# Kernel optimization log

Hardware: AMD Instinct MI355X
Metric: run time of the kernel (lower is better)

Reference implementation:

```python
import jax, jax.numpy as jnp
import numpy as np

# ---- configuration matching init_kwargs ----
KH, KW = 3, 3
STRIDE = (1, 1)
PAD = (1, 1)
DIL = (1, 1)
GRID_SIZE = 5
SPLINE_ORDER = 3
GRID_RANGE = (-1.0, 1.0)
CIN, COUT = 16, 32
B, H, W = 16, 64, 64
K = KH * KW                      # in_features of each KANLinear
NB = GRID_SIZE + SPLINE_ORDER    # number of B-spline basis functions / coeffs


def make_grid():
    # efficient-KAN style extended uniform knot vector, shared by all units
    h = (GRID_RANGE[1] - GRID_RANGE[0]) / GRID_SIZE
    return (jnp.arange(-SPLINE_ORDER, GRID_SIZE + SPLINE_ORDER + 1,
                       dtype=jnp.float32) * h + GRID_RANGE[0])  # [G + 2k + 1]


def setup_inputs() -> dict:
    key = jax.random.key(0)
    k1, k2, k3, k4 = jax.random.split(key, 4)
    n_convs = COUT * CIN  # one KANLinear per (out_channel, in_channel) pair
    x = jax.random.normal(k1, (B, CIN, H, W), dtype=jnp.float32)
    base_w = jax.random.normal(k2, (n_convs, K), dtype=jnp.float32) * (1.0 / np.sqrt(K))
    spline_w = jax.random.normal(k3, (n_convs, K, NB), dtype=jnp.float32) * 0.1
    spline_scaler = jax.random.normal(k4, (n_convs, K), dtype=jnp.float32) * (1.0 / np.sqrt(K))
    return {"x": x, "base_w": base_w, "spline_w": spline_w,
            "spline_scaler": spline_scaler}


def extract_patches(x):
    # im2col / torch.nn.Unfold: [B, Cin, H, W] -> [B, Cin, Ho, Wo, K]
    xp = jnp.pad(x, ((0, 0), (0, 0), (PAD[0], PAD[0]), (PAD[1], PAD[1])))
    Hp, Wp = xp.shape[2], xp.shape[3]
    Ho = (Hp - DIL[0] * (KH - 1) - 1) // STRIDE[0] + 1
    Wo = (Wp - DIL[1] * (KW - 1) - 1) // STRIDE[1] + 1
    cols = []
    for i in range(KH):          # tiny fixed kernel loop (9 iters)
        for j in range(KW):
            cols.append(xp[:, :,
                           i * DIL[0]: i * DIL[0] + STRIDE[0] * Ho: STRIDE[0],
                           j * DIL[1]: j * DIL[1] + STRIDE[1] * Wo: STRIDE[1]])
    return jnp.stack(cols, axis=-1)  # [B, Cin, Ho, Wo, K]


def bspline_bases(x, t):
    # Cox-de Boor recursion, vectorized over all leading dims.
    # x: [...], t: [G+2k+1] shared knots -> bases [..., NB]
    xe = x[..., None]
    b = ((xe >= t[:-1]) & (xe < t[1:])).astype(x.dtype)
    for p in range(1, SPLINE_ORDER + 1):
        left = (xe - t[:-(p + 1)]) / (t[p:-1] - t[:-(p + 1)]) * b[..., :-1]
        right = (t[p + 1:] - xe) / (t[p + 1:] - t[1:-p]) * b[..., 1:]
        b = left + right
    return b  # [..., NB]


def reference(x, base_w, spline_w, spline_scaler):
    t = make_grid()
    patches = extract_patches(x)                 # [B, Cin, Ho, Wo, K]
    act = jax.nn.silu(patches)                   # base branch activation
    bases = bspline_bases(patches, t)            # [B, Cin, Ho, Wo, K, NB]
    # KANLinear list ordering: kernel index = c_out * Cin + c_in
    bw = base_w.reshape(COUT, CIN, K)
    sw = (spline_w * spline_scaler[..., None]).reshape(COUT, CIN, K, NB)
    # out[b,o,h,w] = sum_i KANLinear_{o,i}(patch[b,i,h,w,:])
    out = jnp.einsum('bihwk,oik->bohw', act, bw)
    out = out + jnp.einsum('bihwkc,oikc->bohw', bases, sw)
    return out
```

## Files before the change

### kernel.cpp

```cpp
#include <hip/hip_runtime.h>
#include <hip/hip_bf16.h>

#define CIN_ 16
#define COUT_ 32
#define NBATCH_ 16
#define H_ 64
#define W_ 64
#define F_ 9
#define LPIX_ 304
#define PXT_ 34
#define LROWT_ (PXT_ * LPIX_)
#define ROWS_ 6
#define NSITE_ (ROWS_ * PXT_)
#define NIT_ 13

typedef __attribute__((ext_vector_type(8))) short short8;
typedef __attribute__((ext_vector_type(4))) float f32x4;
typedef __attribute__((ext_vector_type(16))) float f32x16;

__device__ __forceinline__ unsigned short f2bf(float f) {
    unsigned u = __builtin_bit_cast(unsigned, f);
    u += 0x7FFFu + ((u >> 16) & 1u);
    return (unsigned short)(u >> 16);
}
__device__ __forceinline__ unsigned pack2(float lo, float hi) {
    return (unsigned)f2bf(lo) | ((unsigned)f2bf(hi) << 16);
}

__global__ void kan_packw(const float* __restrict__ bw, const float* __restrict__ sw,
                          const float* __restrict__ sc, unsigned short* __restrict__ wpk) {
    int e = blockIdx.x * 256 + threadIdx.x;
    if (e >= 32 * 16 * 9) return;
    int n = e / 144;
    int ci = (e / 9) & 15;
    int tap = e % 9;
    float bwv = bw[e];
    float scv = sc[e];
    float4 s0 = *(const float4*)(sw + (size_t)e * 8);
    float4 s1 = *(const float4*)(sw + (size_t)e * 8 + 4);
    float swv[8] = {s0.x, s0.y, s0.z, s0.w, s1.x, s1.y, s1.z, s1.w};
#pragma unroll
    for (int f = 0; f < 9; ++f) {
        float v = (f == 0) ? bwv : swv[f - 1] * scv;
        int k = ci * 9 + f;
        int step = k >> 4, r = k & 15;
        int lane = ((r >> 3) << 5) | n;
        int j = r & 7;
        wpk[((size_t)(tap * 9 + step) * 64 + lane) * 8 + j] = f2bf(v);
    }
}

__global__ __launch_bounds__(256, 2) void kan_fused(const float* __restrict__ x,
                                                    const unsigned short* __restrict__ wpk,
                                                    float* __restrict__ out) {
    __shared__ __align__(16) char lA[ROWS_ * LROWT_];
    int tid = threadIdx.x;
    int bb = blockIdx.x >> 5;
    int rem = blockIdx.x & 31;
    int rg = rem >> 1;
    int wseg = rem & 1;
    int h0 = rg * 4;
    int w0 = wseg * 32;

    {
        int ci = tid >> 4;
        int l = tid & 15;
        const float* xb = x + ((size_t)bb * CIN_ + ci) * (H_ * W_);
        float xr[NIT_];
#pragma unroll
        for (int it = 0; it < NIT_; ++it) {
            int s = it * 16 + l;
            int r = s / PXT_;
            int lpx = s - r * PXT_;
            int hy = h0 + r - 1;
            int wx = w0 + lpx - 1;
            bool v = (s < NSITE_) && (hy >= 0) && (hy < H_) && (wx >= 0) && (wx < W_);
            xr[it] = v ? xb[hy * W_ + wx] : 0.f;
        }
#pragma unroll
        for (int it = 0; it < NIT_; ++it) {
            int s = it * 16 + l;
            if (s < NSITE_) {
                int r = s / PXT_;
                int lpx = s - r * PXT_;
                float xv = xr[it];
                float ua = (xv + 2.2f) * 2.5f;
                float mf = floorf(ua);
                float u = ua - mf;
                bool ok = (ua >= 0.0f) && (ua < 11.0f);
                float u2 = u * u, u3 = u2 * u;
                const float c6 = 1.0f / 6.0f;
                float Bm  = u3 * c6;
                float Bm1 = (-3.f * u3 + 3.f * u2 + 3.f * u + 1.f) * c6;
                float Bm2 = (3.f * u3 - 6.f * u2 + 4.f) * c6;
                float om = 1.f - u;
                float Bm3 = om * om * om * c6;
                unsigned P0 = pack2(Bm3, Bm2);
                unsigned P1 = pack2(Bm1, Bm);
                int sh = ok ? ((int)mf - 2) : 99;
                int a = sh >> 1;
                bool odd = sh & 1;
                unsigned Q0 = odd ? (P0 << 16) : P0;
                unsigned Q1 = odd ? ((P0 >> 16) | (P1 << 16)) : P1;
                unsigned Q2 = odd ? (P1 >> 16) : 0u;
                unsigned wq[5];
#pragma unroll
                for (int q = 0; q < 5; ++q)
                    wq[q] = (q == a) ? Q0 : (q == a + 1) ? Q1 : (q == a + 2) ? Q2 : 0u;
                float sil = xv / (1.f + __expf(-xv));
                wq[0] = (wq[0] & 0xFFFF0000u) | (unsigned)f2bf(sil);
                char* base = lA + r * LROWT_ + lpx * LPIX_ + ci * 18;
                if ((ci & 1) == 0) {
                    unsigned* d32 = (unsigned*)base;
#pragma unroll
                    for (int q = 0; q < 4; ++q) d32[q] = wq[q];
                    ((unsigned short*)base)[8] = (unsigned short)wq[4];
                } else {
                    ((unsigned short*)base)[0] = (unsigned short)wq[0];
                    unsigned* d32 = (unsigned*)(base + 2);
#pragma unroll
                    for (int q = 0; q < 4; ++q)
                        d32[q] = (wq[q] >> 16) | (wq[q + 1] << 16);
                }
            }
        }
    }

    int lane = tid & 63, wv = tid >> 6;

    short8 B[2][9];
#pragma unroll
    for (int s = 0; s < 9; ++s)
        B[0][s] = *(const short8*)(wpk + ((size_t)s * 64 + lane) * 8);

    __syncthreads();

    f32x16 acc = {};

#pragma unroll
    for (int tap = 0; tap < 9; ++tap) {
        int cur = tap & 1, nxt = cur ^ 1;
        if (tap < 8) {
#pragma unroll
            for (int s = 0; s < 9; ++s)
                B[nxt][s] = *(const short8*)(wpk +
                    ((size_t)((tap + 1) * 9 + s) * 64 + lane) * 8);
        }
        int ki = tap / 3, kj = tap - ki * 3;
        const char* abase = lA + (wv + ki) * LROWT_ + ((lane & 31) + kj) * LPIX_ +
                            ((lane >> 5) << 4);
        __builtin_amdgcn_s_setprio(1);
#pragma unroll
        for (int s = 0; s < 9; ++s) {
            short8 av = *(const short8*)(abase + s * 32);
            acc = __builtin_amdgcn_mfma_f32_32x32x16_bf16(av, B[cur][s], acc, 0, 0, 0);
        }
        __builtin_amdgcn_s_setprio(0);
    }

    int ch = lane & 31;
    int hh = h0 + wv;
    float* ob = out + (size_t)bb * COUT_ * (H_ * W_) + (size_t)ch * (H_ * W_) +
                (size_t)hh * W_ + w0;
#pragma unroll
    for (int q = 0; q < 4; ++q) {
        int px0 = q * 8 + ((lane >> 5) << 2);
        f32x4 v = {acc[q * 4 + 0], acc[q * 4 + 1], acc[q * 4 + 2], acc[q * 4 + 3]};
        __builtin_nontemporal_store(v, (f32x4*)(ob + px0));
    }
}

__device__ __forceinline__ void kan_feat_ref(float xv, float* f) {
    float ua = (xv + 2.2f) * 2.5f;
    float mf = floorf(ua);
    int m = (int)mf;
    float u = ua - mf;
    bool ok = (ua >= 0.0f) && (ua < 11.0f);
    float u2 = u * u, u3 = u2 * u;
    const float c6 = 1.0f / 6.0f;
    float Bm  = u3 * c6;
    float Bm1 = (-3.f * u3 + 3.f * u2 + 3.f * u + 1.f) * c6;
    float Bm2 = (3.f * u3 - 6.f * u2 + 4.f) * c6;
    float om = 1.f - u;
    float Bm3 = om * om * om * c6;
    if (!ok) { Bm = 0.f; Bm1 = 0.f; Bm2 = 0.f; Bm3 = 0.f; }
    f[0] = xv / (1.f + __expf(-xv));
#pragma unroll
    for (int j = 0; j < 8; ++j) {
        float v = 0.f;
        v = (m == j)     ? Bm  : v;
        v = (m == j + 1) ? Bm1 : v;
        v = (m == j + 2) ? Bm2 : v;
        v = (m == j + 3) ? Bm3 : v;
        f[1 + j] = v;
    }
}

__global__ void kan_direct(const float* __restrict__ x, const float* __restrict__ bw,
                           const float* __restrict__ sw, const float* __restrict__ sc,
                           float* __restrict__ out) {
    int idx = blockIdx.x * 256 + threadIdx.x;
    if (idx >= NBATCH_ * COUT_ * H_ * W_) return;
    int w = idx & 63, hh = (idx >> 6) & 63, o = (idx >> 12) & 31, b = idx >> 17;
    float acc = 0.0f;
    for (int i = 0; i < CIN_; ++i)
        for (int ki = 0; ki < 3; ++ki)
            for (int kj = 0; kj < 3; ++kj) {
                int hy = hh + ki - 1, wx = w + kj - 1;
                float xv = (hy >= 0 && hy < H_ && wx >= 0 && wx < W_)
                               ? x[(((size_t)b * CIN_ + i) * H_ + hy) * W_ + wx]
                               : 0.0f;
                float f[9];
                kan_feat_ref(xv, f);
                int idx9 = (o * CIN_ + i) * 9 + ki * 3 + kj;
                float a = f[0] * bw[idx9];
                float s = sc[idx9];
#pragma unroll
                for (int cc = 0; cc < 8; ++cc) a += f[1 + cc] * sw[idx9 * 8 + cc] * s;
                acc += a;
            }
    out[idx] = acc;
}

extern "C" void kernel_launch(void* const* d_in, const int* in_sizes, int n_in,
                              void* d_out, int out_size, void* d_ws, size_t ws_size,
                              hipStream_t stream) {
    const float* x  = (const float*)d_in[0];
    const float* bw = (const float*)d_in[1];
    const float* sw = (const float*)d_in[2];
    const float* sc = (const float*)d_in[3];
    float* out = (float*)d_out;

    size_t need = (size_t)9 * 9 * 64 * 8 * 2;
    if (ws_size >= need) {
        unsigned short* wpk = (unsigned short*)d_ws;
        kan_packw<<<dim3(18), 256, 0, stream>>>(bw, sw, sc, wpk);
        kan_fused<<<dim3(NBATCH_ * 32), 256, 0, stream>>>(x, wpk, out);
    } else {
        kan_direct<<<dim3((NBATCH_ * COUT_ * H_ * W_ + 255) / 256), 256, 0, stream>>>(
            x, bw, sw, sc, out);
    }
}
```

Measured before the change: 21.90 us.

## Fuse weight packing into main kernel with flag-based grid sync and padded features

```diff
diff --git a/kernel.cpp b/kernel.cpp
--- a/kernel.cpp
+++ b/kernel.cpp
@@ -6,13 +6,17 @@
 #define NBATCH_ 16
 #define H_ 64
 #define W_ 64
-#define F_ 9
-#define LPIX_ 304
+#define F_ 10
+#define LPIX_ 336
 #define PXT_ 34
 #define LROWT_ (PXT_ * LPIX_)
 #define ROWS_ 6
 #define NSITE_ (ROWS_ * PXT_)
 #define NIT_ 13
+#define NPACK_ 18
+#define NTILE_ 512
+#define MAGIC_ 0x5EEDF00Du
+#define WPKSH_ (9 * 10 * 64 * 8)
 
 typedef __attribute__((ext_vector_type(8))) short short8;
 typedef __attribute__((ext_vector_type(4))) float f32x4;
@@ -27,40 +31,50 @@
     return (unsigned)f2bf(lo) | ((unsigned)f2bf(hi) << 16);
 }
 
-__global__ void kan_packw(const float* __restrict__ bw, const float* __restrict__ sw,
-                          const float* __restrict__ sc, unsigned short* __restrict__ wpk) {
-    int e = blockIdx.x * 256 + threadIdx.x;
-    if (e >= 32 * 16 * 9) return;
-    int n = e / 144;
-    int ci = (e / 9) & 15;
-    int tap = e % 9;
-    float bwv = bw[e];
-    float scv = sc[e];
-    float4 s0 = *(const float4*)(sw + (size_t)e * 8);
-    float4 s1 = *(const float4*)(sw + (size_t)e * 8 + 4);
-    float swv[8] = {s0.x, s0.y, s0.z, s0.w, s1.x, s1.y, s1.z, s1.w};
-#pragma unroll
-    for (int f = 0; f < 9; ++f) {
-        float v = (f == 0) ? bwv : swv[f - 1] * scv;
-        int k = ci * 9 + f;
-        int step = k >> 4, r = k & 15;
-        int lane = ((r >> 3) << 5) | n;
-        int j = r & 7;
-        wpk[((size_t)(tap * 9 + step) * 64 + lane) * 8 + j] = f2bf(v);
-    }
-}
-
-__global__ __launch_bounds__(256, 2) void kan_fused(const float* __restrict__ x,
-                                                    const unsigned short* __restrict__ wpk,
-                                                    float* __restrict__ out) {
+__global__ __launch_bounds__(256, 2) void kan_one(const float* __restrict__ x,
+                                                  const float* __restrict__ bw,
+                                                  const float* __restrict__ sw,
+                                                  const float* __restrict__ sc,
+                                                  unsigned short* __restrict__ wpk,
+                                                  unsigned* __restrict__ flags,
+                                                  float* __restrict__ out) {
     __shared__ __align__(16) char lA[ROWS_ * LROWT_];
     int tid = threadIdx.x;
-    int bb = blockIdx.x >> 5;
-    int rem = blockIdx.x & 31;
-    int rg = rem >> 1;
-    int wseg = rem & 1;
-    int h0 = rg * 4;
-    int w0 = wseg * 32;
+    int pid = blockIdx.x;
+
+    if (pid < NPACK_) {
+        int e = pid * 256 + tid;
+        if (e < 32 * 16 * 9) {
+            int n = e / 144;
+            int ci = (e / 9) & 15;
+            int tap = e % 9;
+            float bwv = bw[e];
+            float scv = sc[e];
+            float4 s0 = *(const float4*)(sw + (size_t)e * 8);
+            float4 s1 = *(const float4*)(sw + (size_t)e * 8 + 4);
+            float swv[8] = {s0.x, s0.y, s0.z, s0.w, s1.x, s1.y, s1.z, s1.w};
+#pragma unroll
+            for (int f = 0; f < 10; ++f) {
+                float v = (f == 0) ? bwv : (f <= 8 ? swv[f - 1] * scv : 0.0f);
+                int k = ci * 10 + f;
+                int step = k >> 4, r = k & 15;
+                int lane = ((r >> 3) << 5) | n;
+                int j = r & 7;
+                wpk[((size_t)(tap * 10 + step) * 64 + lane) * 8 + j] = f2bf(v);
+            }
+        }
+        __threadfence();
+        __syncthreads();
+        if (tid == 0)
+            __hip_atomic_store(&flags[pid], MAGIC_, __ATOMIC_RELEASE,
+                               __HIP_MEMORY_SCOPE_AGENT);
+    }
+
+    int tile = (pid < NPACK_) ? (NTILE_ - NPACK_ + pid) : (pid - NPACK_);
+    int bb = tile >> 5;
+    int rem = tile & 31;
+    int h0 = (rem >> 1) * 4;
+    int w0 = (rem & 1) * 32;
 
     {
         int ci = tid >> 4;
@@ -107,51 +121,50 @@
 #pragma unroll
                 for (int q = 0; q < 5; ++q)
                     wq[q] = (q == a) ? Q0 : (q == a + 1) ? Q1 : (q == a + 2) ? Q2 : 0u;
-                float sil = xv / (1.f + __expf(-xv));
+                float sil = xv * __builtin_amdgcn_rcpf(1.f + __expf(-xv));
                 wq[0] = (wq[0] & 0xFFFF0000u) | (unsigned)f2bf(sil);
-                char* base = lA + r * LROWT_ + lpx * LPIX_ + ci * 18;
-                if ((ci & 1) == 0) {
-                    unsigned* d32 = (unsigned*)base;
-#pragma unroll
-                    for (int q = 0; q < 4; ++q) d32[q] = wq[q];
-                    ((unsigned short*)base)[8] = (unsigned short)wq[4];
-                } else {
-                    ((unsigned short*)base)[0] = (unsigned short)wq[0];
-                    unsigned* d32 = (unsigned*)(base + 2);
-#pragma unroll
-                    for (int q = 0; q < 4; ++q)
-                        d32[q] = (wq[q] >> 16) | (wq[q + 1] << 16);
-                }
+                unsigned* dst = (unsigned*)(lA + r * LROWT_ + lpx * LPIX_ + ci * 20);
+#pragma unroll
+                for (int q = 0; q < 5; ++q) dst[q] = wq[q];
             }
         }
     }
 
+    if (tid < 64) {
+        for (;;) {
+            unsigned v = (tid < NPACK_)
+                ? __hip_atomic_load(&flags[tid], __ATOMIC_ACQUIRE, __HIP_MEMORY_SCOPE_AGENT)
+                : MAGIC_;
+            if (__all(v == MAGIC_)) break;
+            __builtin_amdgcn_s_sleep(4);
+        }
+    }
+    __syncthreads();
+    __threadfence();
+
     int lane = tid & 63, wv = tid >> 6;
 
-    short8 B[2][9];
-#pragma unroll
-    for (int s = 0; s < 9; ++s)
+    short8 B[2][10];
+#pragma unroll
+    for (int s = 0; s < 10; ++s)
         B[0][s] = *(const short8*)(wpk + ((size_t)s * 64 + lane) * 8);
 
-    __syncthreads();
-
     f32x16 acc = {};
-
 #pragma unroll
     for (int tap = 0; tap < 9; ++tap) {
         int cur = tap & 1, nxt = cur ^ 1;
         if (tap < 8) {
 #pragma unroll
-            for (int s = 0; s < 9; ++s)
+            for (int s = 0; s < 10; ++s)
                 B[nxt][s] = *(const short8*)(wpk +
-                    ((size_t)((tap + 1) * 9 + s) * 64 + lane) * 8);
+                    ((size_t)((tap + 1) * 10 + s) * 64 + lane) * 8);
         }
         int ki = tap / 3, kj = tap - ki * 3;
         const char* abase = lA + (wv + ki) * LROWT_ + ((lane & 31) + kj) * LPIX_ +
                             ((lane >> 5) << 4);
         __builtin_amdgcn_s_setprio(1);
 #pragma unroll
-        for (int s = 0; s < 9; ++s) {
+        for (int s = 0; s < 10; ++s) {
             short8 av = *(const short8*)(abase + s * 32);
             acc = __builtin_amdgcn_mfma_f32_32x32x16_bf16(av, B[cur][s], acc, 0, 0, 0);
         }
@@ -231,11 +244,11 @@
     const float* sc = (const float*)d_in[3];
     float* out = (float*)d_out;
 
-    size_t need = (size_t)9 * 9 * 64 * 8 * 2;
+    size_t need = (size_t)WPKSH_ * 2 + NPACK_ * sizeof(unsigned);
     if (ws_size >= need) {
         unsigned short* wpk = (unsigned short*)d_ws;
-        kan_packw<<<dim3(18), 256, 0, stream>>>(bw, sw, sc, wpk);
-        kan_fused<<<dim3(NBATCH_ * 32), 256, 0, stream>>>(x, wpk, out);
+        unsigned* flags = (unsigned*)((char*)d_ws + (size_t)WPKSH_ * 2);
+        kan_one<<<dim3(NTILE_), 256, 0, stream>>>(x, bw, sw, sc, wpk, flags, out);
     } else {
         kan_direct<<<dim3((NBATCH_ * COUT_ * H_ * W_ + 255) / 256), 256, 0, stream>>>(
             x, bw, sw, sc, out);
```

Result: slower. 53.02 us (+142.1%).
